# Kernel optimization log

Hardware: AMD Instinct MI355X
Metric: run time of the kernel (lower is better)

Reference implementation:

```python
import jax, jax.numpy as jnp
import numpy as np

N, E, C = 50000, 800000, 100000
D_IN, HID = 128, 128
MLP_IN, MLP_HID = 2 * HID + 1, HID // 2
BN_EPS = 1e-5
NEG_SLOPE = 0.01


def setup_inputs() -> dict:
    key = jax.random.key(0)
    ks = jax.random.split(key, 24)
    inp = {
        "x": jax.random.normal(ks[0], (N, D_IN), jnp.float32),
        "src": jax.random.randint(ks[1], (E,), 0, N, jnp.int32),
        "dst": jax.random.randint(ks[2], (E,), 0, N, jnp.int32),
        "cand_u": jax.random.randint(ks[3], (C,), 0, N, jnp.int32),
        "cand_v": jax.random.randint(ks[4], (C,), 0, N, jnp.int32),
        "cand_feat": jax.random.normal(ks[5], (C, 1), jnp.float32),
    }
    s = 1.0 / np.sqrt(D_IN)
    # SAGEConv layer 0 and 1 (in=out=128 since statedim == pnhid)
    for li, k0 in [(0, 6), (1, 12)]:
        inp[f"w_self{li}"] = jax.random.uniform(ks[k0], (D_IN, HID), jnp.float32, -s, s)
        inp[f"w_neigh{li}"] = jax.random.uniform(ks[k0 + 1], (D_IN, HID), jnp.float32, -s, s)
        inp[f"b{li}"] = jnp.zeros((HID,), jnp.float32)
        inp[f"gamma{li}"] = jnp.ones((HID,), jnp.float32)
        inp[f"beta{li}"] = jnp.zeros((HID,), jnp.float32)
        inp[f"rm{li}"] = jax.random.normal(ks[k0 + 2], (HID,), jnp.float32) * 0.1
        inp[f"rv{li}"] = jax.random.uniform(ks[k0 + 3], (HID,), jnp.float32, 0.5, 1.5)
    # confidence MLP: 257 -> 64 -> 64 -> 1
    sizes = [MLP_IN, MLP_HID, MLP_HID, 1]
    for i in range(3):
        si = 1.0 / np.sqrt(sizes[i])
        inp[f"mw{i}"] = jax.random.uniform(ks[18 + 2 * i], (sizes[i], sizes[i + 1]), jnp.float32, -si, si)
        inp[f"mb{i}"] = jax.random.uniform(ks[19 + 2 * i], (sizes[i + 1],), jnp.float32, -si, si)
    return inp


def _sage_bn_block(x, src, dst, w_self, w_neigh, b, gamma, beta, rm, rv):
    # mean aggregation over incoming edges (gather -> scatter-add -> divide)
    msgs = x[src]  # [E, D]
    agg = jax.ops.segment_sum(msgs, dst, num_segments=N)  # [N, D]
    deg = jax.ops.segment_sum(jnp.ones((src.shape[0],), x.dtype), dst, num_segments=N)
    agg = agg / jnp.maximum(deg, 1.0)[:, None]
    h = x @ w_self + agg @ w_neigh + b
    # BatchNorm1d (eval mode, running stats) then leaky_relu; dropout is identity in eval
    h = gamma * (h - rm) * jax.lax.rsqrt(rv + BN_EPS) + beta
    return jax.nn.leaky_relu(h, NEG_SLOPE)


def reference(x, src, dst, cand_u, cand_v, cand_feat,
              w_self0, w_neigh0, b0, gamma0, beta0, rm0, rv0,
              w_self1, w_neigh1, b1, gamma1, beta1, rm1, rv1,
              mw0, mb0, mw1, mb1, mw2, mb2):
    h = _sage_bn_block(x, src, dst, w_self0, w_neigh0, b0, gamma0, beta0, rm0, rv0)
    h = _sage_bn_block(h, src, dst, w_self1, w_neigh1, b1, gamma1, beta1, rm1, rv1)
    h = jnp.nan_to_num(h, nan=1e-14)
    # candidate embeddings: [C, 2*HID + 1]
    ce = jnp.concatenate([h[cand_u], h[cand_v], cand_feat], axis=-1)
    z = jax.nn.leaky_relu(ce @ mw0 + mb0, NEG_SLOPE)
    z = jax.nn.leaky_relu(z @ mw1 + mb1, NEG_SLOPE)
    y = z @ mw2 + mb2  # [C, 1]
    return y, jax.nn.softmax(y, axis=0)
```

## Files before the change

kernel.cpp:

```cpp
#include <hip/hip_runtime.h>
#include <math.h>

#define N_NODES 50000
#define N_EDGES 800000
#define N_CAND  100000
#define D       128
#define BN_EPS  1e-5f
#define SLOPE   0.01f

#define NB2     196
#define TILE    4096
#define NTILE   196
#define BCAP    4736

typedef __attribute__((ext_vector_type(8))) short bf16x8;
typedef __attribute__((ext_vector_type(4))) float f32x4;

__device__ __forceinline__ float lrelu(float x){ return x >= 0.f ? x : SLOPE * x; }

__device__ __forceinline__ unsigned short f2bf_rn(float f){
  unsigned int u = __float_as_uint(f);
  unsigned int r = u + 0x7FFFu + ((u >> 16) & 1u);
  return (unsigned short)(r >> 16);
}
__device__ __forceinline__ float bf2f(unsigned short h){
  return __uint_as_float(((unsigned int)h) << 16);
}
__device__ __forceinline__ float bfu(unsigned u){ return __uint_as_float(u << 16); }
__device__ __forceinline__ float bfh(unsigned u){ return __uint_as_float(u & 0xffff0000u); }
__device__ __forceinline__ float4 bf4f(ushort4 u){
  return make_float4(__uint_as_float((unsigned)u.x << 16),
                     __uint_as_float((unsigned)u.y << 16),
                     __uint_as_float((unsigned)u.z << 16),
                     __uint_as_float((unsigned)u.w << 16));
}

__device__ __forceinline__ unsigned pk_bf16(float a, float b){
  unsigned r;
  asm("v_cvt_pk_bf16_f32 %0, %1, %2" : "=v"(r) : "v"(a), "v"(b));
  return r;
}
__device__ __forceinline__ void split2(float a, float b, unsigned &h, unsigned &l){
  h = pk_bf16(a, b);
  float ra = a - __uint_as_float(h << 16);
  float rb = b - __uint_as_float(h & 0xffff0000u);
  l = pk_bf16(ra, rb);
}

__global__ __launch_bounds__(256) void k_bin(const int* __restrict__ src, const int* __restrict__ dst,
                                             int* __restrict__ gcnt, unsigned* __restrict__ ebin, int E){
  __shared__ unsigned stage[TILE];
  __shared__ int hist[256], lscan[256], lex[256], lcur[256], gbase[256];
  __shared__ int stot;
  int t = threadIdx.x;
  int e0 = blockIdx.x * TILE;

  hist[t] = 0;
  __syncthreads();

  unsigned pk[16]; int bk[16]; bool ok[16];
  #pragma unroll
  for (int j = 0; j < 16; ++j){
    int i = e0 + j * 256 + t;
    ok[j] = (i < E);
    if (ok[j]){
      int d = dst[i];
      pk[j] = ((unsigned)d << 16) | (unsigned)src[i];
      bk[j] = d >> 8;
      atomicAdd(&hist[bk[j]], 1);
    }
  }
  __syncthreads();

  lscan[t] = hist[t];
  __syncthreads();
  for (int off = 1; off < 256; off <<= 1){
    int v = (t >= off) ? lscan[t - off] : 0;
    __syncthreads();
    lscan[t] += v;
    __syncthreads();
  }
  int ex = lscan[t] - hist[t];
  lex[t]  = ex;
  lcur[t] = ex;
  if (t < NB2) gbase[t] = hist[t] ? atomicAdd(&gcnt[t], hist[t]) : 0;
  if (t == 255) stot = lscan[255];
  __syncthreads();

  #pragma unroll
  for (int j = 0; j < 16; ++j){
    if (ok[j]){
      int p = atomicAdd(&lcur[bk[j]], 1);
      stage[p] = pk[j];
    }
  }
  __syncthreads();

  int tot = stot;
  for (int i = t; i < tot; i += 256){
    unsigned e = stage[i];
    int b = (int)(e >> 24);
    ebin[(size_t)b * BCAP + gbase[b] + (i - lex[b])] = e;
  }
}

__global__ __launch_bounds__(256) void k_bscan2(const int* __restrict__ gcnt, int* __restrict__ bbase,
                                                int* __restrict__ rowptr){
  __shared__ int sd[256];
  int t = threadIdx.x;
  int v = (t < NB2) ? gcnt[t] : 0;
  sd[t] = v; __syncthreads();
  for (int off = 1; off < 256; off <<= 1){
    int a = (t >= off) ? sd[t - off] : 0;
    __syncthreads();
    sd[t] += a; __syncthreads();
  }
  if (t < NB2) bbase[t] = sd[t] - v;
  if (t == NB2 - 1) rowptr[N_NODES] = sd[t];
}

__global__ __launch_bounds__(256) void k_bfin(const int* __restrict__ gcnt, const int* __restrict__ bbase,
                                              const unsigned* __restrict__ ebin,
                                              unsigned short* __restrict__ eid16,
                                              int* __restrict__ rowptr, int n){
  __shared__ int hist[256], lb[256], lcur[256];
  int t = threadIdx.x, b = blockIdx.x;
  int cb   = gcnt[b];
  int base = bbase[b];
  const unsigned* eb = &ebin[(size_t)b * BCAP];
  hist[t] = 0;
  __syncthreads();
  for (int idx = t; idx < cb; idx += 256) atomicAdd(&hist[(eb[idx] >> 16) & 255], 1);
  __syncthreads();
  lb[t] = hist[t];
  __syncthreads();
  for (int off = 1; off < 256; off <<= 1){
    int v = (t >= off) ? lb[t - off] : 0;
    __syncthreads();
    lb[t] += v; __syncthreads();
  }
  int ex = lb[t] - hist[t];
  lcur[t] = ex;
  int node = (b << 8) + t;
  if (node < n) rowptr[node] = base + ex;
  __syncthreads();
  for (int idx = t; idx < cb; idx += 256){
    unsigned e = eb[idx];
    int p = atomicAdd(&lcur[(e >> 16) & 255], 1);
    eid16[base + p] = (unsigned short)(e & 0xffffu);
  }
}

__global__ __launch_bounds__(256) void k_prep(
    const float* __restrict__ ws0, const float* __restrict__ wn0,
    const float* __restrict__ ws1, const float* __restrict__ wn1,
    const float* __restrict__ mw0, const float* __restrict__ mw1,
    const float* __restrict__ X,
    unsigned short* __restrict__ bth0, unsigned short* __restrict__ btl0,
    unsigned short* __restrict__ bth1, unsigned short* __restrict__ btl1,
    unsigned short* __restrict__ w1th, unsigned short* __restrict__ w1tl,
    unsigned short* __restrict__ w0cth, unsigned short* __restrict__ w0ctl,
    unsigned short* __restrict__ XH, unsigned short* __restrict__ XL)
{
  int b = blockIdx.x, t = threadIdx.x;
  if (b < 256){
    int col = b & 127;
    const float* wsp = (b < 128) ? ws0 : ws1;
    const float* wnp = (b < 128) ? wn0 : wn1;
    unsigned short* th = (b < 128) ? bth0 : bth1;
    unsigned short* tl = (b < 128) ? btl0 : btl1;
    float v = (t < 128) ? wsp[t * D + col] : wnp[(t - 128) * D + col];
    unsigned short hi = f2bf_rn(v);
    th[col * 256 + t] = hi;
    tl[col * 256 + t] = f2bf_rn(v - bf2f(hi));
  } else if (b < 320){
    if (t < 64){
      int col = b - 256;
      float v = mw1[t * 64 + col];
      unsigned short hi = f2bf_rn(v);
      w1th[col * 64 + t] = hi;
      w1tl[col * 64 + t] = f2bf_rn(v - bf2f(hi));
    }
  } else if (b < 448){
    if (t < 128){
      int col = b - 320;
      float v = (col < 64) ? mw0[t * 64 + col] : mw0[(128 + t) * 64 + (col - 64)];
      unsigned short hi = f2bf_rn(v);
      w0cth[col * 128 + t] = hi;
      w0ctl[col * 128 + t] = f2bf_rn(v - bf2f(hi));
    }
  } else {
    int i = (b - 448) * 256 + t;
    if (i < N_NODES * D / 8){
      const float4* xp = reinterpret_cast<const float4*>(&X[(size_t)i * 8]);
      float4 v0 = xp[0], v1 = xp[1];
      uint4 h, l;
      split2(v0.x, v0.y, h.x, l.x);
      split2(v0.z, v0.w, h.y, l.y);
      split2(v1.x, v1.y, h.z, l.z);
      split2(v1.z, v1.w, h.w, l.w);
      *reinterpret_cast<uint4*>(&XH[(size_t)i * 8]) = h;
      *reinterpret_cast<uint4*>(&XL[(size_t)i * 8]) = l;
    }
  }
}

__global__ __launch_bounds__(256) void k_agg_bf(const unsigned short* __restrict__ XB,
                                                const int* __restrict__ rowptr, const unsigned short* __restrict__ eid,
                                                unsigned short* __restrict__ AGH, unsigned short* __restrict__ AGL,
                                                int n){
  int g = blockIdx.x * 8 + (threadIdx.x >> 5);
  int l = threadIdx.x & 31;
  if (g >= n) return;
  int e0 = rowptr[g], e1 = rowptr[g + 1];
  float4 a0 = make_float4(0.f,0.f,0.f,0.f);
  float4 a1 = make_float4(0.f,0.f,0.f,0.f);
  float4 a2 = make_float4(0.f,0.f,0.f,0.f);
  float4 a3 = make_float4(0.f,0.f,0.f,0.f);
  int e = e0;
  for (; e + 4 <= e1; e += 4){
    int s0 = eid[e], s1 = eid[e + 1], s2 = eid[e + 2], s3 = eid[e + 3];
    ushort4 u0 = *reinterpret_cast<const ushort4*>(&XB[(size_t)s0 * D + l * 4]);
    ushort4 u1 = *reinterpret_cast<const ushort4*>(&XB[(size_t)s1 * D + l * 4]);
    ushort4 u2 = *reinterpret_cast<const ushort4*>(&XB[(size_t)s2 * D + l * 4]);
    ushort4 u3 = *reinterpret_cast<const ushort4*>(&XB[(size_t)s3 * D + l * 4]);
    float4 f0 = bf4f(u0), f1 = bf4f(u1), f2 = bf4f(u2), f3 = bf4f(u3);
    a0.x += f0.x; a0.y += f0.y; a0.z += f0.z; a0.w += f0.w;
    a1.x += f1.x; a1.y += f1.y; a1.z += f1.z; a1.w += f1.w;
    a2.x += f2.x; a2.y += f2.y; a2.z += f2.z; a2.w += f2.w;
    a3.x += f3.x; a3.y += f3.y; a3.z += f3.z; a3.w += f3.w;
  }
  for (; e < e1; ++e){
    int s0 = eid[e];
    ushort4 u0 = *reinterpret_cast<const ushort4*>(&XB[(size_t)s0 * D + l * 4]);
    float4 f0 = bf4f(u0);
    a0.x += f0.x; a0.y += f0.y; a0.z += f0.z; a0.w += f0.w;
  }
  float sc = 1.f / fmaxf((float)(e1 - e0), 1.f);
  float ox = (a0.x + a1.x + a2.x + a3.x) * sc;
  float oy = (a0.y + a1.y + a2.y + a3.y) * sc;
  float oz = (a0.z + a1.z + a2.z + a3.z) * sc;
  float ow = (a0.w + a1.w + a2.w + a3.w) * sc;
  uint2 h, lo_;
  split2(ox, oy, h.x, lo_.x);
  split2(oz, ow, h.y, lo_.y);
  *reinterpret_cast<uint2*>(&AGH[(size_t)g * D + l * 4]) = h;
  *reinterpret_cast<uint2*>(&AGL[(size_t)g * D + l * 4]) = lo_;
}

__global__ __launch_bounds__(256) void k_sage_mfma(
    const unsigned short* __restrict__ A0H, const unsigned short* __restrict__ A0L,
    const unsigned short* __restrict__ A1H, const unsigned short* __restrict__ A1L,
    const unsigned short* __restrict__ BTH, const unsigned short* __restrict__ BTL,
    const float* __restrict__ Bb, const float* __restrict__ GM, const float* __restrict__ BT,
    const float* __restrict__ RM, const float* __restrict__ RV,
    unsigned short* __restrict__ HBH, unsigned short* __restrict__ HBL,
    int n, int donan)
{
  __shared__ unsigned short Ah[64 * 40];
  __shared__ unsigned short Al[64 * 40];
  __shared__ unsigned short Bh[128 * 40];
  __shared__ unsigned short Bl[128 * 40];

  int t  = threadIdx.x;
  int l  = t & 63;
  int wv = t >> 6;
  int lm = l & 15;
  int lk = l >> 4;
  int node0 = blockIdx.x * 64;

  f32x4 acc[8];
  #pragma unroll
  for (int f = 0; f < 8; ++f) acc[f] = (f32x4){0.f, 0.f, 0.f, 0.f};

  for (int step = 0; step < 8; ++step){
    int k0 = step * 32;
    const unsigned short* srcH = (step < 4) ? A0H : A1H;
    const unsigned short* srcL = (step < 4) ? A0L : A1L;
    int koff = (step < 4) ? k0 : (k0 - 128);

    __syncthreads();
    {
      int row = t >> 2, q = t & 3;
      int node = min(node0 + row, n - 1);
      *reinterpret_cast<uint4*>(&Ah[row * 40 + q * 8]) =
          *reinterpret_cast<const uint4*>(&srcH[(size_t)node * D + koff + q * 8]);
      *reinterpret_cast<uint4*>(&Al[row * 40 + q * 8]) =
          *reinterpret_cast<const uint4*>(&srcL[(size_t)node * D + koff + q * 8]);
    }
    #pragma unroll
    for (int i = 0; i < 2; ++i){
      int c   = t + i * 256;
      int col = c >> 2, q = c & 3;
      *reinterpret_cast<uint4*>(&Bh[col * 40 + q * 8]) =
          *reinterpret_cast<const uint4*>(&BTH[col * 256 + k0 + q * 8]);
      *reinterpret_cast<uint4*>(&Bl[col * 40 + q * 8]) =
          *reinterpret_cast<const uint4*>(&BTL[col * 256 + k0 + q * 8]);
    }
    __syncthreads();

    bf16x8 afh = *reinterpret_cast<const bf16x8*>(&Ah[(wv * 16 + lm) * 40 + lk * 8]);
    bf16x8 afl = *reinterpret_cast<const bf16x8*>(&Al[(wv * 16 + lm) * 40 + lk * 8]);
    #pragma unroll
    for (int f = 0; f < 8; ++f){
      bf16x8 bfh = *reinterpret_cast<const bf16x8*>(&Bh[(f * 16 + lm) * 40 + lk * 8]);
      bf16x8 bfl = *reinterpret_cast<const bf16x8*>(&Bl[(f * 16 + lm) * 40 + lk * 8]);
      acc[f] = __builtin_amdgcn_mfma_f32_16x16x32_bf16(afh, bfh, acc[f], 0, 0, 0);
      acc[f] = __builtin_amdgcn_mfma_f32_16x16x32_bf16(afl, bfh, acc[f], 0, 0, 0);
      acc[f] = __builtin_amdgcn_mfma_f32_16x16x32_bf16(afh, bfl, acc[f], 0, 0, 0);
    }
  }

  #pragma unroll
  for (int f = 0; f < 8; ++f){
    int col = f * 16 + lm;
    float s  = GM[col] * rsqrtf(RV[col] + BN_EPS);
    float cj = (Bb[col] - RM[col]) * s + BT[col];
    #pragma unroll
    for (int r = 0; r < 4; ++r){
      int node = node0 + wv * 16 + lk * 4 + r;
      if (node < n){
        float v = lrelu(acc[f][r] * s + cj);
        if (donan && (v != v)) v = 1e-14f;
        unsigned short h16 = f2bf_rn(v);
        HBH[(size_t)node * D + col] = h16;
        HBL[(size_t)node * D + col] = f2bf_rn(v - bf2f(h16));
      }
    }
  }
}

__global__ __launch_bounds__(256) void k_pgemm(
    const unsigned short* __restrict__ HH, const unsigned short* __restrict__ HL,
    const unsigned short* __restrict__ WCH, const unsigned short* __restrict__ WCL,
    unsigned short* __restrict__ PH, unsigned short* __restrict__ PL, int n)
{
  __shared__ unsigned short Ah[64 * 40];
  __shared__ unsigned short Al[64 * 40];
  __shared__ unsigned short Bh[128 * 40];
  __shared__ unsigned short Bl[128 * 40];

  int t  = threadIdx.x;
  int l  = t & 63;
  int wv = t >> 6;
  int lm = l & 15;
  int lk = l >> 4;
  int node0 = blockIdx.x * 64;

  f32x4 acc[8];
  #pragma unroll
  for (int f = 0; f < 8; ++f) acc[f] = (f32x4){0.f, 0.f, 0.f, 0.f};

  for (int step = 0; step < 4; ++step){
    int k0 = step * 32;
    __syncthreads();
    {
      int row = t >> 2, q = t & 3;
      int node = min(node0 + row, n - 1);
      *reinterpret_cast<uint4*>(&Ah[row * 40 + q * 8]) =
          *reinterpret_cast<const uint4*>(&HH[(size_t)node * D + k0 + q * 8]);
      *reinterpret_cast<uint4*>(&Al[row * 40 + q * 8]) =
          *reinterpret_cast<const uint4*>(&HL[(size_t)node * D + k0 + q * 8]);
    }
    #pragma unroll
    for (int i = 0; i < 2; ++i){
      int c = t + i * 256;
      int col = c >> 2, q = c & 3;
      *reinterpret_cast<uint4*>(&Bh[col * 40 + q * 8]) =
          *reinterpret_cast<const uint4*>(&WCH[col * 128 + k0 + q * 8]);
      *reinterpret_cast<uint4*>(&Bl[col * 40 + q * 8]) =
          *reinterpret_cast<const uint4*>(&WCL[col * 128 + k0 + q * 8]);
    }
    __syncthreads();

    bf16x8 afh = *reinterpret_cast<const bf16x8*>(&Ah[(wv * 16 + lm) * 40 + lk * 8]);
    bf16x8 afl = *reinterpret_cast<const bf16x8*>(&Al[(wv * 16 + lm) * 40 + lk * 8]);
    #pragma unroll
    for (int f = 0; f < 8; ++f){
      bf16x8 bfh = *reinterpret_cast<const bf16x8*>(&Bh[(f * 16 + lm) * 40 + lk * 8]);
      bf16x8 bfl = *reinterpret_cast<const bf16x8*>(&Bl[(f * 16 + lm) * 40 + lk * 8]);
      acc[f] = __builtin_amdgcn_mfma_f32_16x16x32_bf16(afh, bfh, acc[f], 0, 0, 0);
      acc[f] = __builtin_amdgcn_mfma_f32_16x16x32_bf16(afl, bfh, acc[f], 0, 0, 0);
      acc[f] = __builtin_amdgcn_mfma_f32_16x16x32_bf16(afh, bfl, acc[f], 0, 0, 0);
    }
  }

  #pragma unroll
  for (int f = 0; f < 8; ++f){
    int col = f * 16 + lm;
    #pragma unroll
    for (int r = 0; r < 4; ++r){
      int node = node0 + wv * 16 + lk * 4 + r;
      if (node < n){
        float v = acc[f][r];
        unsigned short h16 = f2bf_rn(v);
        PH[(size_t)node * D + col] = h16;
        PL[(size_t)node * D + col] = f2bf_rn(v - bf2f(h16));
      }
    }
  }
}

__device__ __forceinline__ void proc2(unsigned uh, unsigned ul, unsigned vh, unsigned vl,
                                      float wfa, float wfb, float b0a, float b0b, float cfv,
                                      unsigned &ho, unsigned &lo_){
  float z0 = lrelu(bfu(uh) + bfu(ul) + bfu(vh) + bfu(vl) + cfv * wfa + b0a);
  float z1 = lrelu(bfh(uh) + bfh(ul) + bfh(vh) + bfh(vl) + cfv * wfb + b0b);
  split2(z0, z1, ho, lo_);
}

__global__ __launch_bounds__(256) void k_mlp2(
    const unsigned short* __restrict__ PH, const unsigned short* __restrict__ PL,
    const int* __restrict__ cu, const int* __restrict__ cv, const float* __restrict__ cf,
    const float* __restrict__ mw0, const float* __restrict__ mb0,
    const unsigned short* __restrict__ W1H, const unsigned short* __restrict__ W1L,
    const float* __restrict__ mb1, const float* __restrict__ mw2, const float* __restrict__ mb2,
    float* __restrict__ y, int C)
{
  __shared__ unsigned short zh[4][32 * 72];
  __shared__ unsigned short zl[4][32 * 72];
  __shared__ float bw[64], ww[64];

  int t = threadIdx.x;
  int wv = t >> 6, l = t & 63, lm = l & 15, lk = l >> 4;
  int cl = l & 31, hsel = l >> 5;
  int candbase = blockIdx.x * 128 + wv * 32;

  if (t < 64){ bw[t] = mb0[t]; ww[t] = mw0[256 * 64 + t]; }
  __syncthreads();

  int cc = min(candbase + cl, C - 1);
  int nu = cu[cc], nv = cv[cc];
  float cfv = cf[cc];

  const uint4* puh = reinterpret_cast<const uint4*>(&PH[(size_t)nu * D + hsel * 32]);
  const uint4* pul = reinterpret_cast<const uint4*>(&PL[(size_t)nu * D + hsel * 32]);
  const uint4* pvh = reinterpret_cast<const uint4*>(&PH[(size_t)nv * D + 64 + hsel * 32]);
  const uint4* pvl = reinterpret_cast<const uint4*>(&PL[(size_t)nv * D + 64 + hsel * 32]);
  uint4 uh0 = puh[0], uh1 = puh[1], uh2 = puh[2], uh3 = puh[3];
  uint4 ul0 = pul[0], ul1 = pul[1], ul2 = pul[2], ul3 = pul[3];
  uint4 vh0 = pvh[0], vh1 = pvh[1], vh2 = pvh[2], vh3 = pvh[3];
  uint4 vl0 = pvl[0], vl1 = pvl[1], vl2 = pvl[2], vl3 = pvl[3];

  int colb = hsel * 32;
  unsigned short* zhr = &zh[wv][cl * 72];
  unsigned short* zlr = &zl[wv][cl * 72];
  #define PROC_W(UH, UL, VH, VL, CO) { \
    unsigned ho, lo_; \
    proc2(UH, UL, VH, VL, ww[colb + (CO)], ww[colb + (CO) + 1], bw[colb + (CO)], bw[colb + (CO) + 1], cfv, ho, lo_); \
    *reinterpret_cast<unsigned*>(&zhr[colb + (CO)]) = ho; \
    *reinterpret_cast<unsigned*>(&zlr[colb + (CO)]) = lo_; }
  PROC_W(uh0.x, ul0.x, vh0.x, vl0.x, 0)  PROC_W(uh0.y, ul0.y, vh0.y, vl0.y, 2)
  PROC_W(uh0.z, ul0.z, vh0.z, vl0.z, 4)  PROC_W(uh0.w, ul0.w, vh0.w, vl0.w, 6)
  PROC_W(uh1.x, ul1.x, vh1.x, vl1.x, 8)  PROC_W(uh1.y, ul1.y, vh1.y, vl1.y, 10)
  PROC_W(uh1.z, ul1.z, vh1.z, vl1.z, 12) PROC_W(uh1.w, ul1.w, vh1.w, vl1.w, 14)
  PROC_W(uh2.x, ul2.x, vh2.x, vl2.x, 16) PROC_W(uh2.y, ul2.y, vh2.y, vl2.y, 18)
  PROC_W(uh2.z, ul2.z, vh2.z, vl2.z, 20) PROC_W(uh2.w, ul2.w, vh2.w, vl2.w, 22)
  PROC_W(uh3.x, ul3.x, vh3.x, vl3.x, 24) PROC_W(uh3.y, ul3.y, vh3.y, vl3.y, 26)
  PROC_W(uh3.z, ul3.z, vh3.z, vl3.z, 28) PROC_W(uh3.w, ul3.w, vh3.w, vl3.w, 30)
  #undef PROC_W

  int kbase = lk * 8;
  f32x4 a2[2][4];
  #pragma unroll
  for (int m = 0; m < 2; ++m)
    #pragma unroll
    for (int f = 0; f < 4; ++f) a2[m][f] = (f32x4){0.f, 0.f, 0.f, 0.f};

  #pragma unroll
  for (int s2 = 0; s2 < 2; ++s2){
    int kk = s2 * 32 + kbase;
    bf16x8 azh0 = *reinterpret_cast<const bf16x8*>(&zh[wv][(0 * 16 + lm) * 72 + kk]);
    bf16x8 azl0 = *reinterpret_cast<const bf16x8*>(&zl[wv][(0 * 16 + lm) * 72 + kk]);
    bf16x8 azh1 = *reinterpret_cast<const bf16x8*>(&zh[wv][(1 * 16 + lm) * 72 + kk]);
    bf16x8 azl1 = *reinterpret_cast<const bf16x8*>(&zl[wv][(1 * 16 + lm) * 72 + kk]);
    #pragma unroll
    for (int f = 0; f < 4; ++f){
      int col = f * 16 + lm;
      bf16x8 bh = *reinterpret_cast<const bf16x8*>(&W1H[(size_t)col * 64 + kk]);
      bf16x8 bl = *reinterpret_cast<const bf16x8*>(&W1L[(size_t)col * 64 + kk]);
      a2[0][f] = __builtin_amdgcn_mfma_f32_16x16x32_bf16(azh0, bh, a2[0][f], 0, 0, 0);
      a2[0][f] = __builtin_amdgcn_mfma_f32_16x16x32_bf16(azl0, bh, a2[0][f], 0, 0, 0);
      a2[0][f] = __builtin_amdgcn_mfma_f32_16x16x32_bf16(azh0, bl, a2[0][f], 0, 0, 0);
      a2[1][f] = __builtin_amdgcn_mfma_f32_16x16x32_bf16(azh1, bh, a2[1][f], 0, 0, 0);
      a2[1][f] = __builtin_amdgcn_mfma_f32_16x16x32_bf16(azl1, bh, a2[1][f], 0, 0, 0);
      a2[1][f] = __builtin_amdgcn_mfma_f32_16x16x32_bf16(azh1, bl, a2[1][f], 0, 0, 0);
    }
  }

  float p00 = 0.f, p01 = 0.f, p02 = 0.f, p03 = 0.f;
  float p10 = 0.f, p11 = 0.f, p12 = 0.f, p13 = 0.f;
  #pragma unroll
  for (int f = 0; f < 4; ++f){
    int col = f * 16 + lm;
    float b1v = mb1[col];
    float w2v = mw2[col];
    p00 = fmaf(lrelu(a2[0][f][0] + b1v), w2v, p00);
    p01 = fmaf(lrelu(a2[0][f][1] + b1v), w2v, p01);
    p02 = fmaf(lrelu(a2[0][f][2] + b1v), w2v, p02);
    p03 = fmaf(lrelu(a2[0][f][3] + b1v), w2v, p03);
    p10 = fmaf(lrelu(a2[1][f][0] + b1v), w2v, p10);
    p11 = fmaf(lrelu(a2[1][f][1] + b1v), w2v, p11);
    p12 = fmaf(lrelu(a2[1][f][2] + b1v), w2v, p12);
    p13 = fmaf(lrelu(a2[1][f][3] + b1v), w2v, p13);
  }
  #pragma unroll
  for (int off = 1; off < 16; off <<= 1){
    p00 += __shfl_xor(p00, off); p01 += __shfl_xor(p01, off);
    p02 += __shfl_xor(p02, off); p03 += __shfl_xor(p03, off);
    p10 += __shfl_xor(p10, off); p11 += __shfl_xor(p11, off);
    p12 += __shfl_xor(p12, off); p13 += __shfl_xor(p13, off);
  }
  if (lm == 0){
    float b2 = mb2[0];
    int base0 = candbase + lk * 4;
    int base1 = candbase + 16 + lk * 4;
    if (base0 + 0 < C) y[base0 + 0] = p00 + b2;
    if (base0 + 1 < C) y[base0 + 1] = p01 + b2;
    if (base0 + 2 < C) y[base0 + 2] = p02 + b2;
    if (base0 + 3 < C) y[base0 + 3] = p03 + b2;
    if (base1 + 0 < C) y[base1 + 0] = p10 + b2;
    if (base1 + 1 < C) y[base1 + 1] = p11 + b2;
    if (base1 + 2 < C) y[base1 + 2] = p12 + b2;
    if (base1 + 3 < C) y[base1 + 3] = p13 + b2;
  }
}

__global__ __launch_bounds__(256) void k_red1(const float* __restrict__ y,
                                              float* __restrict__ bmax, float* __restrict__ bsum, int C){
  __shared__ float sm[4];
  __shared__ float ss[4];
  int t = threadIdx.x;
  float m = -3.4e38f;
  for (int i = blockIdx.x * 256 + t; i < C; i += gridDim.x * 256) m = fmaxf(m, y[i]);
  for (int o = 32; o; o >>= 1) m = fmaxf(m, __shfl_xor(m, o));
  if ((t & 63) == 0) sm[t >> 6] = m;
  __syncthreads();
  float bm = fmaxf(fmaxf(sm[0], sm[1]), fmaxf(sm[2], sm[3]));
  float s = 0.f;
  for (int i = blockIdx.x * 256 + t; i < C; i += gridDim.x * 256) s += expf(y[i] - bm);
  for (int o = 32; o; o >>= 1) s += __shfl_xor(s, o);
  if ((t & 63) == 0) ss[t >> 6] = s;
  __syncthreads();
  if (t == 0){ bmax[blockIdx.x] = bm; bsum[blockIdx.x] = ss[0] + ss[1] + ss[2] + ss[3]; }
}

__global__ __launch_bounds__(256) void k_red2(const float* __restrict__ bmax, const float* __restrict__ bsum,
                                              float* __restrict__ g, int nb){
  __shared__ float sm[4];
  __shared__ float ss[4];
  int t = threadIdx.x;
  float m0 = (t < nb) ? bmax[t] : -3.4e38f;
  float m = m0;
  for (int o = 32; o; o >>= 1) m = fmaxf(m, __shfl_xor(m, o));
  if ((t & 63) == 0) sm[t >> 6] = m;
  __syncthreads();
  float gm = fmaxf(fmaxf(sm[0], sm[1]), fmaxf(sm[2], sm[3]));
  float s = (t < nb) ? bsum[t] * expf(m0 - gm) : 0.f;
  for (int o = 32; o; o >>= 1) s += __shfl_xor(s, o);
  if ((t & 63) == 0) ss[t >> 6] = s;
  __syncthreads();
  if (t == 0){ g[0] = gm; g[1] = 1.f / (ss[0] + ss[1] + ss[2] + ss[3]); }
}

__global__ __launch_bounds__(256) void k_red3(const float* __restrict__ y, const float* __restrict__ g,
                                              float* __restrict__ out, int C){
  int i = blockIdx.x * 256 + threadIdx.x;
  if (i < C) out[i] = expf(y[i] - g[0]) * g[1];
}

extern "C" void kernel_launch(void* const* d_in, const int* in_sizes, int n_in,
                              void* d_out, int out_size, void* d_ws, size_t ws_size,
                              hipStream_t stream)
{
  const float* x   = (const float*)d_in[0];
  const int*   src = (const int*)  d_in[1];
  const int*   dst = (const int*)  d_in[2];
  const int*   cu  = (const int*)  d_in[3];
  const int*   cv  = (const int*)  d_in[4];
  const float* cf  = (const float*)d_in[5];
  const float* ws0 = (const float*)d_in[6];
  const float* wn0 = (const float*)d_in[7];
  const float* b0  = (const float*)d_in[8];
  const float* g0  = (const float*)d_in[9];
  const float* be0 = (const float*)d_in[10];
  const float* rm0 = (const float*)d_in[11];
  const float* rv0 = (const float*)d_in[12];
  const float* ws1 = (const float*)d_in[13];
  const float* wn1 = (const float*)d_in[14];
  const float* b1  = (const float*)d_in[15];
  const float* g1  = (const float*)d_in[16];
  const float* be1 = (const float*)d_in[17];
  const float* rm1 = (const float*)d_in[18];
  const float* rv1 = (const float*)d_in[19];
  const float* mw0 = (const float*)d_in[20];
  const float* mb0 = (const float*)d_in[21];
  const float* mw1 = (const float*)d_in[22];
  const float* mb1 = (const float*)d_in[23];
  const float* mw2 = (const float*)d_in[24];
  const float* mb2 = (const float*)d_in[25];

  float* out = (float*)d_out;

  char* w = (char*)d_ws;
  char* regA = w; w += (size_t)N_NODES * D * 4;
  char* regB = w; w += (size_t)N_NODES * D * 4;
  char* regC = w; w += (size_t)N_NODES * D * 4;
  int* cnt     = (int*)w;   w += (size_t)N_NODES * 4;
  int* rowptr  = (int*)w;   w += (size_t)(N_NODES + 1) * 4;
  int* cur     = (int*)w;   w += (size_t)N_NODES * 4;
  int* eid     = (int*)w;   w += (size_t)N_EDGES * 4;
  int* gcnt    = (int*)w;   w += (size_t)(NB2 + 8) * 4;
  int* bbase   = (int*)w;   w += (size_t)(NB2 + 1) * 4;
  float* bmax  = (float*)w; w += 256 * 4;
  float* bsumF = (float*)w; w += 256 * 4;
  float* gred  = (float*)w; w += 2 * 4;
  unsigned short* w1th  = (unsigned short*)w; w += (size_t)64 * 64 * 2;
  unsigned short* w1tl  = (unsigned short*)w; w += (size_t)64 * 64 * 2;
  unsigned short* w0cth = (unsigned short*)w; w += (size_t)128 * 128 * 2;
  unsigned short* w0ctl = (unsigned short*)w; w += (size_t)128 * 128 * 2;

  unsigned short* eid16 = (unsigned short*)eid;

  unsigned* ebin = (unsigned*)regB;
  unsigned short* hb0h = (unsigned short*)regB;
  unsigned short* hb0l = hb0h + (size_t)N_NODES * D;
  unsigned short* xh   = (unsigned short*)regC;
  unsigned short* xl   = xh + (size_t)N_NODES * D;
  unsigned short* hb1h = (unsigned short*)regC;
  unsigned short* hb1l = hb1h + (size_t)N_NODES * D;
  unsigned short* agh = (unsigned short*)regA;
  unsigned short* agl = agh + (size_t)N_NODES * D;
  unsigned short* pbh = (unsigned short*)regA;
  unsigned short* pbl = pbh + (size_t)N_NODES * D;

  unsigned short* bth0 = (unsigned short*)cnt;
  unsigned short* btl0 = bth0 + 128 * 256;
  unsigned short* bth1 = (unsigned short*)cur;
  unsigned short* btl1 = bth1 + 128 * 256;

  hipMemsetAsync(gcnt, 0, (size_t)NB2 * 4, stream);
  k_bin   <<<NTILE, 256, 0, stream>>>(src, dst, gcnt, ebin, N_EDGES);
  k_bscan2<<<1, 256, 0, stream>>>(gcnt, bbase, rowptr);
  k_bfin  <<<NB2, 256, 0, stream>>>(gcnt, bbase, ebin, eid16, rowptr, N_NODES);

  int PREPB = 448 + (N_NODES * D / 8 + 255) / 256;
  k_prep<<<PREPB, 256, 0, stream>>>(ws0, wn0, ws1, wn1, mw0, mw1, x,
      bth0, btl0, bth1, btl1, w1th, w1tl, w0cth, w0ctl, xh, xl);

  int GB = (N_NODES + 63) / 64;
  k_agg_bf<<<(N_NODES + 7) / 8, 256, 0, stream>>>(xh, rowptr, eid16, agh, agl, N_NODES);
  k_sage_mfma<<<GB, 256, 0, stream>>>(xh, xl, agh, agl, bth0, btl0,
                                      b0, g0, be0, rm0, rv0, hb0h, hb0l, N_NODES, 0);
  k_agg_bf<<<(N_NODES + 7) / 8, 256, 0, stream>>>(hb0h, rowptr, eid16, agh, agl, N_NODES);
  k_sage_mfma<<<GB, 256, 0, stream>>>(hb0h, hb0l, agh, agl, bth1, btl1,
                                      b1, g1, be1, rm1, rv1, hb1h, hb1l, N_NODES, 1);

  k_pgemm<<<GB, 256, 0, stream>>>(hb1h, hb1l, w0cth, w0ctl, pbh, pbl, N_NODES);

  k_mlp2<<<(N_CAND + 127) / 128, 256, 0, stream>>>(pbh, pbl, cu, cv, cf,
      mw0, mb0, w1th, w1tl, mb1, mw2, mb2, out, N_CAND);

  k_red1<<<256, 256, 0, stream>>>(out, bmax, bsumF, N_CAND);
  k_red2<<<1, 256, 0, stream>>>(bmax, bsumF, gred, 256);
  k_red3<<<(N_CAND + 255) / 256, 256, 0, stream>>>(out, gred, out + N_CAND, N_CAND);
}
```

Baseline: 210.1 us.

## Fuse softmax partial reduction into MLP, widen aggregation loads, halve bin tiles

The per-block softmax max/sum partials are now computed inside the MLP kernel from shared memory, which removes the separate k_red1 pass that re-read all outputs. k_red2 is widened to handle up to 1024 partials. The aggregation kernel now uses 16 lanes per node with 16-byte loads instead of 32 lanes with 8-byte loads. The binning kernel uses half-size tiles across twice as many blocks. The cost is more block partials to combine and fewer threads per node in the gather.

```diff
diff --git a/kernel.cpp b/kernel.cpp
--- a/kernel.cpp
+++ b/kernel.cpp
@@ -9,9 +9,11 @@
 #define SLOPE   0.01f
 
 #define NB2     196
-#define TILE    4096
-#define NTILE   196
+#define TILE    2048
+#define NTILE   391
 #define BCAP    4736
+
+#define MLPB    782
 
 typedef __attribute__((ext_vector_type(8))) short bf16x8;
 typedef __attribute__((ext_vector_type(4))) float f32x4;
@@ -28,12 +30,6 @@
 }
 __device__ __forceinline__ float bfu(unsigned u){ return __uint_as_float(u << 16); }
 __device__ __forceinline__ float bfh(unsigned u){ return __uint_as_float(u & 0xffff0000u); }
-__device__ __forceinline__ float4 bf4f(ushort4 u){
-  return make_float4(__uint_as_float((unsigned)u.x << 16),
-                     __uint_as_float((unsigned)u.y << 16),
-                     __uint_as_float((unsigned)u.z << 16),
-                     __uint_as_float((unsigned)u.w << 16));
-}
 
 __device__ __forceinline__ unsigned pk_bf16(float a, float b){
   unsigned r;
@@ -45,6 +41,12 @@
   float ra = a - __uint_as_float(h << 16);
   float rb = b - __uint_as_float(h & 0xffff0000u);
   l = pk_bf16(ra, rb);
+}
+__device__ __forceinline__ void acc8(const uint4 &u, float* a){
+  a[0] += bfu(u.x); a[1] += bfh(u.x);
+  a[2] += bfu(u.y); a[3] += bfh(u.y);
+  a[4] += bfu(u.z); a[5] += bfh(u.z);
+  a[6] += bfu(u.w); a[7] += bfh(u.w);
 }
 
 __global__ __launch_bounds__(256) void k_bin(const int* __restrict__ src, const int* __restrict__ dst,
@@ -58,9 +60,9 @@
   hist[t] = 0;
   __syncthreads();
 
-  unsigned pk[16]; int bk[16]; bool ok[16];
-  #pragma unroll
-  for (int j = 0; j < 16; ++j){
+  unsigned pk[8]; int bk[8]; bool ok[8];
+  #pragma unroll
+  for (int j = 0; j < 8; ++j){
     int i = e0 + j * 256 + t;
     ok[j] = (i < E);
     if (ok[j]){
@@ -88,7 +90,7 @@
   __syncthreads();
 
   #pragma unroll
-  for (int j = 0; j < 16; ++j){
+  for (int j = 0; j < 8; ++j){
     if (ok[j]){
       int p = atomicAdd(&lcur[bk[j]], 1);
       stage[p] = pk[j];
@@ -209,43 +211,37 @@
                                                 const int* __restrict__ rowptr, const unsigned short* __restrict__ eid,
                                                 unsigned short* __restrict__ AGH, unsigned short* __restrict__ AGL,
                                                 int n){
-  int g = blockIdx.x * 8 + (threadIdx.x >> 5);
-  int l = threadIdx.x & 31;
+  int g = blockIdx.x * 16 + (threadIdx.x >> 4);
+  int l = threadIdx.x & 15;
   if (g >= n) return;
   int e0 = rowptr[g], e1 = rowptr[g + 1];
-  float4 a0 = make_float4(0.f,0.f,0.f,0.f);
-  float4 a1 = make_float4(0.f,0.f,0.f,0.f);
-  float4 a2 = make_float4(0.f,0.f,0.f,0.f);
-  float4 a3 = make_float4(0.f,0.f,0.f,0.f);
+  float a0[8] = {}, a1[8] = {}, a2[8] = {}, a3[8] = {};
+  int off = l * 8;
   int e = e0;
   for (; e + 4 <= e1; e += 4){
     int s0 = eid[e], s1 = eid[e + 1], s2 = eid[e + 2], s3 = eid[e + 3];
-    ushort4 u0 = *reinterpret_cast<const ushort4*>(&XB[(size_t)s0 * D + l * 4]);
-    ushort4 u1 = *reinterpret_cast<const ushort4*>(&XB[(size_t)s1 * D + l * 4]);
-    ushort4 u2 = *reinterpret_cast<const ushort4*>(&XB[(size_t)s2 * D + l * 4]);
-    ushort4 u3 = *reinterpret_cast<const ushort4*>(&XB[(size_t)s3 * D + l * 4]);
-    float4 f0 = bf4f(u0), f1 = bf4f(u1), f2 = bf4f(u2), f3 = bf4f(u3);
-    a0.x += f0.x; a0.y += f0.y; a0.z += f0.z; a0.w += f0.w;
-    a1.x += f1.x; a1.y += f1.y; a1.z += f1.z; a1.w += f1.w;
-    a2.x += f2.x; a2.y += f2.y; a2.z += f2.z; a2.w += f2.w;
-    a3.x += f3.x; a3.y += f3.y; a3.z += f3.z; a3.w += f3.w;
+    uint4 u0 = *reinterpret_cast<const uint4*>(&XB[(size_t)s0 * D + off]);
+    uint4 u1 = *reinterpret_cast<const uint4*>(&XB[(size_t)s1 * D + off]);
+    uint4 u2 = *reinterpret_cast<const uint4*>(&XB[(size_t)s2 * D + off]);
+    uint4 u3 = *reinterpret_cast<const uint4*>(&XB[(size_t)s3 * D + off]);
+    acc8(u0, a0); acc8(u1, a1); acc8(u2, a2); acc8(u3, a3);
   }
   for (; e < e1; ++e){
     int s0 = eid[e];
-    ushort4 u0 = *reinterpret_cast<const ushort4*>(&XB[(size_t)s0 * D + l * 4]);
-    float4 f0 = bf4f(u0);
-    a0.x += f0.x; a0.y += f0.y; a0.z += f0.z; a0.w += f0.w;
+    uint4 u0 = *reinterpret_cast<const uint4*>(&XB[(size_t)s0 * D + off]);
+    acc8(u0, a0);
   }
   float sc = 1.f / fmaxf((float)(e1 - e0), 1.f);
-  float ox = (a0.x + a1.x + a2.x + a3.x) * sc;
-  float oy = (a0.y + a1.y + a2.y + a3.y) * sc;
-  float oz = (a0.z + a1.z + a2.z + a3.z) * sc;
-  float ow = (a0.w + a1.w + a2.w + a3.w) * sc;
-  uint2 h, lo_;
-  split2(ox, oy, h.x, lo_.x);
-  split2(oz, ow, h.y, lo_.y);
-  *reinterpret_cast<uint2*>(&AGH[(size_t)g * D + l * 4]) = h;
-  *reinterpret_cast<uint2*>(&AGL[(size_t)g * D + l * 4]) = lo_;
+  uint4 h, lo_;
+  unsigned* hp = (unsigned*)&h; unsigned* lp = (unsigned*)&lo_;
+  #pragma unroll
+  for (int j = 0; j < 4; ++j){
+    float va = (a0[2*j]   + a1[2*j]   + a2[2*j]   + a3[2*j])   * sc;
+    float vb = (a0[2*j+1] + a1[2*j+1] + a2[2*j+1] + a3[2*j+1]) * sc;
+    split2(va, vb, hp[j], lp[j]);
+  }
+  *reinterpret_cast<uint4*>(&AGH[(size_t)g * D + off]) = h;
+  *reinterpret_cast<uint4*>(&AGL[(size_t)g * D + off]) = lo_;
 }
 
 __global__ __launch_bounds__(256) void k_sage_mfma(
@@ -415,11 +411,13 @@
     const float* __restrict__ mw0, const float* __restrict__ mb0,
     const unsigned short* __restrict__ W1H, const unsigned short* __restrict__ W1L,
     const float* __restrict__ mb1, const float* __restrict__ mw2, const float* __restrict__ mb2,
-    float* __restrict__ y, int C)
+    float* __restrict__ y, float* __restrict__ bmax, float* __restrict__ bsum, int C)
 {
   __shared__ unsigned short zh[4][32 * 72];
   __shared__ unsigned short zl[4][32 * 72];
   __shared__ float bw[64], ww[64];
+  __shared__ float ys[128];
+  __shared__ float sm[4], ss[4];
 
   int t = threadIdx.x;
   int wv = t >> 6, l = t & 63, lm = l & 15, lk = l >> 4;
@@ -427,6 +425,7 @@
   int candbase = blockIdx.x * 128 + wv * 32;
 
   if (t < 64){ bw[t] = mb0[t]; ww[t] = mw0[256 * 64 + t]; }
+  if (t < 128) ys[t] = -3.4e38f;
   __syncthreads();
 
   int cc = min(candbase + cl, C - 1);
@@ -515,30 +514,24 @@
     float b2 = mb2[0];
     int base0 = candbase + lk * 4;
     int base1 = candbase + 16 + lk * 4;
-    if (base0 + 0 < C) y[base0 + 0] = p00 + b2;
-    if (base0 + 1 < C) y[base0 + 1] = p01 + b2;
-    if (base0 + 2 < C) y[base0 + 2] = p02 + b2;
-    if (base0 + 3 < C) y[base0 + 3] = p03 + b2;
-    if (base1 + 0 < C) y[base1 + 0] = p10 + b2;
-    if (base1 + 1 < C) y[base1 + 1] = p11 + b2;
-    if (base1 + 2 < C) y[base1 + 2] = p12 + b2;
-    if (base1 + 3 < C) y[base1 + 3] = p13 + b2;
-  }
-}
-
-__global__ __launch_bounds__(256) void k_red1(const float* __restrict__ y,
-                                              float* __restrict__ bmax, float* __restrict__ bsum, int C){
-  __shared__ float sm[4];
-  __shared__ float ss[4];
-  int t = threadIdx.x;
-  float m = -3.4e38f;
-  for (int i = blockIdx.x * 256 + t; i < C; i += gridDim.x * 256) m = fmaxf(m, y[i]);
+    int lb0 = wv * 32 + lk * 4;
+    if (base0 + 0 < C){ y[base0 + 0] = p00 + b2; ys[lb0 + 0] = p00 + b2; }
+    if (base0 + 1 < C){ y[base0 + 1] = p01 + b2; ys[lb0 + 1] = p01 + b2; }
+    if (base0 + 2 < C){ y[base0 + 2] = p02 + b2; ys[lb0 + 2] = p02 + b2; }
+    if (base0 + 3 < C){ y[base0 + 3] = p03 + b2; ys[lb0 + 3] = p03 + b2; }
+    if (base1 + 0 < C){ y[base1 + 0] = p10 + b2; ys[lb0 + 16] = p10 + b2; }
+    if (base1 + 1 < C){ y[base1 + 1] = p11 + b2; ys[lb0 + 17] = p11 + b2; }
+    if (base1 + 2 < C){ y[base1 + 2] = p12 + b2; ys[lb0 + 18] = p12 + b2; }
+    if (base1 + 3 < C){ y[base1 + 3] = p13 + b2; ys[lb0 + 19] = p13 + b2; }
+  }
+  __syncthreads();
+
+  float m = (t < 128) ? ys[t] : -3.4e38f;
   for (int o = 32; o; o >>= 1) m = fmaxf(m, __shfl_xor(m, o));
   if ((t & 63) == 0) sm[t >> 6] = m;
   __syncthreads();
   float bm = fmaxf(fmaxf(sm[0], sm[1]), fmaxf(sm[2], sm[3]));
-  float s = 0.f;
-  for (int i = blockIdx.x * 256 + t; i < C; i += gridDim.x * 256) s += expf(y[i] - bm);
+  float s = (t < 128 && ys[t] > -3.3e38f) ? expf(ys[t] - bm) : 0.f;
   for (int o = 32; o; o >>= 1) s += __shfl_xor(s, o);
   if ((t & 63) == 0) ss[t >> 6] = s;
   __syncthreads();
@@ -550,13 +543,22 @@
   __shared__ float sm[4];
   __shared__ float ss[4];
   int t = threadIdx.x;
-  float m0 = (t < nb) ? bmax[t] : -3.4e38f;
-  float m = m0;
+  float m0[4]; float s0[4];
+  #pragma unroll
+  for (int j = 0; j < 4; ++j){
+    int i = t + j * 256;
+    m0[j] = (i < nb) ? bmax[i] : -3.4e38f;
+    s0[j] = (i < nb) ? bsum[i] : 0.f;
+  }
+  float m = fmaxf(fmaxf(m0[0], m0[1]), fmaxf(m0[2], m0[3]));
   for (int o = 32; o; o >>= 1) m = fmaxf(m, __shfl_xor(m, o));
   if ((t & 63) == 0) sm[t >> 6] = m;
   __syncthreads();
   float gm = fmaxf(fmaxf(sm[0], sm[1]), fmaxf(sm[2], sm[3]));
-  float s = (t < nb) ? bsum[t] * expf(m0 - gm) : 0.f;
+  float s = 0.f;
+  #pragma unroll
+  for (int j = 0; j < 4; ++j)
+    if (m0[j] > -3.3e38f) s += s0[j] * expf(m0[j] - gm);
   for (int o = 32; o; o >>= 1) s += __shfl_xor(s, o);
   if ((t & 63) == 0) ss[t >> 6] = s;
   __syncthreads();
@@ -612,8 +614,8 @@
   int* eid     = (int*)w;   w += (size_t)N_EDGES * 4;
   int* gcnt    = (int*)w;   w += (size_t)(NB2 + 8) * 4;
   int* bbase   = (int*)w;   w += (size_t)(NB2 + 1) * 4;
-  float* bmax  = (float*)w; w += 256 * 4;
-  float* bsumF = (float*)w; w += 256 * 4;
+  float* bmax  = (float*)w; w += (size_t)(MLPB + 8) * 4;
+  float* bsumF = (float*)w; w += (size_t)(MLPB + 8) * 4;
   float* gred  = (float*)w; w += 2 * 4;
   unsigned short* w1th  = (unsigned short*)w; w += (size_t)64 * 64 * 2;
   unsigned short* w1tl  = (unsigned short*)w; w += (size_t)64 * 64 * 2;
@@ -649,19 +651,19 @@
       bth0, btl0, bth1, btl1, w1th, w1tl, w0cth, w0ctl, xh, xl);
 
   int GB = (N_NODES + 63) / 64;
-  k_agg_bf<<<(N_NODES + 7) / 8, 256, 0, stream>>>(xh, rowptr, eid16, agh, agl, N_NODES);
+  int AB = (N_NODES + 15) / 16;
+  k_agg_bf<<<AB, 256, 0, stream>>>(xh, rowptr, eid16, agh, agl, N_NODES);
   k_sage_mfma<<<GB, 256, 0, stream>>>(xh, xl, agh, agl, bth0, btl0,
                                       b0, g0, be0, rm0, rv0, hb0h, hb0l, N_NODES, 0);
-  k_agg_bf<<<(N_NODES + 7) / 8, 256, 0, stream>>>(hb0h, rowptr, eid16, agh, agl, N_NODES);
+  k_agg_bf<<<AB, 256, 0, stream>>>(hb0h, rowptr, eid16, agh, agl, N_NODES);
   k_sage_mfma<<<GB, 256, 0, stream>>>(hb0h, hb0l, agh, agl, bth1, btl1,
                                       b1, g1, be1, rm1, rv1, hb1h, hb1l, N_NODES, 1);
 
   k_pgemm<<<GB, 256, 0, stream>>>(hb1h, hb1l, w0cth, w0ctl, pbh, pbl, N_NODES);
 
-  k_mlp2<<<(N_CAND + 127) / 128, 256, 0, stream>>>(pbh, pbl, cu, cv, cf,
-      mw0, mb0, w1th, w1tl, mb1, mw2, mb2, out, N_CAND);
-
-  k_red1<<<256, 256, 0, stream>>>(out, bmax, bsumF, N_CAND);
-  k_red2<<<1, 256, 0, stream>>>(bmax, bsumF, gred, 256);
+  k_mlp2<<<MLPB, 256, 0, stream>>>(pbh, pbl, cu, cv, cf,
+      mw0, mb0, w1th, w1tl, mb1, mw2, mb2, out, bmax, bsumF, N_CAND);
+
+  k_red2<<<1, 256, 0, stream>>>(bmax, bsumF, gred, MLPB);
   k_red3<<<(N_CAND + 255) / 256, 256, 0, stream>>>(out, gred, out + N_CAND, N_CAND);
 }
```

Result: no change. 211.0 us (+0.4%).
